# Optimization experiments

Hardware: AMD Instinct MI355X
Metric: run time of the kernel (lower is better)

## Reference

```python
import jax, jax.numpy as jnp
import numpy as np

P, IMG, CH, DM, NL = 16, 224, 3, 512, 6
DI, N, K, R = 2 * DM, 16, 4, DM // 16  # d_inner, d_state, d_conv, dt_rank
BATCH = 32
L = (IMG // P) ** 2
PD = CH * P * P


def layernorm(x, g, b, eps=1e-5):
    mu = x.mean(-1, keepdims=True)
    var = x.var(-1, keepdims=True)
    return (x - mu) / jnp.sqrt(var + eps) * g + b


def mamba_layer(x, inW, convW, convB, xpW, dtW, dtB, A_log, Dvec, outW):
    # x: (B, L, DM)
    Bsz, Ls, _ = x.shape
    xz = x @ inW.T                      # (B, L, 2*DI), in_proj (bias=False)
    xs, z = jnp.split(xz, 2, axis=-1)   # (B, L, DI) each
    # causal depthwise conv1d (kernel K, left pad K-1, truncate to L)
    xp = jnp.pad(xs, ((0, 0), (K - 1, 0), (0, 0)))
    xc = sum(convW[:, k] * xp[:, k:k + Ls, :] for k in range(K)) + convB
    xc = jax.nn.silu(xc)
    # input-dependent dt, B, C
    x_dbl = xc @ xpW.T                  # (B, L, R + 2N)
    dt, Bm, Cm = jnp.split(x_dbl, [R, R + N], axis=-1)
    dt = jax.nn.softplus(dt @ dtW.T + dtB)  # (B, L, DI)
    A = -jnp.exp(A_log)                 # (DI, N)

    def step(h, inp):
        xt, dtt, Bt, Ct = inp           # (B,DI),(B,DI),(B,N),(B,N)
        dA = jnp.exp(dtt[:, :, None] * A)              # (B, DI, N)
        h = dA * h + dtt[:, :, None] * Bt[:, None, :] * xt[:, :, None]
        y = jnp.einsum('bdn,bn->bd', h, Ct)
        return h, y

    h0 = jnp.zeros((Bsz, DI, N), xs.dtype)
    xs_t = jnp.swapaxes(xc, 0, 1)
    dt_t = jnp.swapaxes(dt, 0, 1)
    B_t = jnp.swapaxes(Bm, 0, 1)
    C_t = jnp.swapaxes(Cm, 0, 1)
    _, ys = jax.lax.scan(step, h0, (xs_t, dt_t, B_t, C_t))
    y = jnp.swapaxes(ys, 0, 1) + xc * Dvec   # skip term D*x
    y = y * jax.nn.silu(z)
    return y @ outW.T                    # out_proj (bias=False)


def setup_inputs() -> dict:
    key = jax.random.key(0)
    ks = jax.random.split(key, 16)
    s = 0.02
    inp = {
        'x': jax.random.normal(ks[0], (BATCH, CH, IMG, IMG), jnp.float32),
        'ln0_g': jnp.ones((PD,), jnp.float32),
        'ln0_b': jnp.zeros((PD,), jnp.float32),
        'W_emb': jax.random.normal(ks[1], (DM, PD), jnp.float32) * s,
        'b_emb': jnp.zeros((DM,), jnp.float32),
        'ln1_g': jnp.ones((DM,), jnp.float32),
        'ln1_b': jnp.zeros((DM,), jnp.float32),
        'in_proj_w': jax.random.normal(ks[2], (NL, 2 * DI, DM), jnp.float32) * s,
        'conv_w': jax.random.normal(ks[3], (NL, DI, K), jnp.float32) * 0.1,
        'conv_b': jnp.zeros((NL, DI), jnp.float32),
        'x_proj_w': jax.random.normal(ks[4], (NL, R + 2 * N, DI), jnp.float32) * s,
        'dt_proj_w': jax.random.normal(ks[5], (NL, DI, R), jnp.float32) * s,
        'dt_proj_b': jnp.full((NL, DI), float(np.log(np.expm1(0.01))), jnp.float32),
        'A_log': jnp.tile(jnp.log(jnp.arange(1, N + 1, dtype=jnp.float32)), (NL, DI, 1)),
        'D_p': jnp.ones((NL, DI), jnp.float32),
        'out_proj_w': jax.random.normal(ks[6], (NL, DM, DI), jnp.float32) * s,
        'blk_ln_g': jnp.ones((NL, DM), jnp.float32),
        'blk_ln_b': jnp.zeros((NL, DM), jnp.float32),
        'W_head': jax.random.normal(ks[7], (10, DM), jnp.float32) * s,
        'b_head': jnp.zeros((10,), jnp.float32),
    }
    return inp


def reference(x, ln0_g, ln0_b, W_emb, b_emb, ln1_g, ln1_b, in_proj_w, conv_w,
              conv_b, x_proj_w, dt_proj_w, dt_proj_b, A_log, D_p, out_proj_w,
              blk_ln_g, blk_ln_b, W_head, b_head):
    B = x.shape[0]
    # patchify: b c (h p1) (w p2) -> b (h w) (c p1 p2)
    g = IMG // P
    t = x.reshape(B, CH, g, P, g, P).transpose(0, 2, 4, 1, 3, 5).reshape(B, g * g, PD)
    t = layernorm(t, ln0_g, ln0_b)
    t = t @ W_emb.T + b_emb
    t = layernorm(t, ln1_g, ln1_b)
    for i in range(NL):
        y = mamba_layer(t, in_proj_w[i], conv_w[i], conv_b[i], x_proj_w[i],
                        dt_proj_w[i], dt_proj_b[i], A_log[i], D_p[i], out_proj_w[i])
        t = layernorm(y + t, blk_ln_g[i], blk_ln_b[i])
    pooled = t.mean(axis=1)
    return pooled @ W_head.T + b_head
```

## Files before the change

kernel.cpp:

```cpp
#include <hip/hip_runtime.h>
#include <cstdint>
#include <cstddef>

#define BATCHN 32
#define LSEQ   196
#define DMODEL 512
#define DINNER 1024
#define PDIM   768
#define NSTATE 16
#define RRANK  32
#define NLAYER 6

typedef __bf16 bf16_t;
typedef __bf16 bf16x8 __attribute__((ext_vector_type(8)));
typedef float  f32x4  __attribute__((ext_vector_type(4)));

__device__ __forceinline__ void gl_lds16(const bf16_t* g, bf16_t* l) {
    __builtin_amdgcn_global_load_lds(
        (const __attribute__((address_space(1))) void*)g,
        (__attribute__((address_space(3))) void*)l, 16, 0, 0);
}

__device__ __forceinline__ size_t swz_addr(int row, int c, int KT) {
    return (((size_t)(row >> 4) * KT + (c >> 5)) << 9)
         + (((row & 15) | (((c >> 3) & 3) << 4)) << 3) + (c & 7);
}

__global__ __launch_bounds__(256) void split_kernel(
    const float* __restrict__ src, bf16_t* __restrict__ hi,
    bf16_t* __restrict__ lo, int n)
{
    int i = blockIdx.x * 256 + threadIdx.x;
    if (i < n) {
        float x = src[i];
        bf16_t h = (bf16_t)x;
        hi[i] = h;
        lo[i] = (bf16_t)(x - (float)h);
    }
}

__global__ __launch_bounds__(256) void gemm_mfma3(
    const bf16_t* __restrict__ Ah, const bf16_t* __restrict__ Al,
    const bf16_t* __restrict__ Wh, const bf16_t* __restrict__ Wl,
    float* __restrict__ C, const float* __restrict__ bias,
    int M, int N, int K)
{
    __shared__ bf16_t sBh[2][128 * 32];
    __shared__ bf16_t sBl[2][128 * 32];

    const int bm = blockIdx.y * 128;
    const int bn = blockIdx.x * 128;
    const int kchunk = K / gridDim.z;
    const int kb = blockIdx.z * kchunk;
    const int KT = K >> 5;
    C += (size_t)blockIdx.z * M * N;

    const int tid  = threadIdx.x;
    const int lane = tid & 63;
    const int w    = tid >> 6;
    const int wm   = (w & 1) * 64;
    const int wn   = (w >> 1) * 64;

    const int lrow = lane >> 2;
    const int cg8  = ((lane & 3) ^ ((lane >> 3) & 3)) * 8;
    const size_t brow = (size_t)(bn + w * 32 + lrow) * K + cg8;
    const int llo = w * 1024;

    const int fr  = lane & 15;
    const int fsw = ((lane >> 4) ^ ((lane >> 1) & 3)) * 8;

    const size_t abase = ((size_t)((bm + wm) >> 4) * KT + (kb >> 5)) * 512
                       + (size_t)lane * 8;
    const size_t amt = (size_t)KT * 512;

    f32x4 acc[4][4] = {};

    #pragma unroll
    for (int j = 0; j < 2; ++j) {
        gl_lds16(Wh + brow + (size_t)j * 16 * K + kb, &sBh[0][llo + j * 512]);
        gl_lds16(Wl + brow + (size_t)j * 16 * K + kb, &sBl[0][llo + j * 512]);
    }
    bf16x8 afh[4], afl[4];
    #pragma unroll
    for (int mt = 0; mt < 4; ++mt) {
        afh[mt] = *(const bf16x8*)(Ah + abase + (size_t)mt * amt);
        afl[mt] = *(const bf16x8*)(Al + abase + (size_t)mt * amt);
    }

    const int kiter = kchunk / 32;
    for (int ki = 0; ki < kiter; ++ki) {
        const int buf = ki & 1;
        __syncthreads();

        bf16x8 nfh[4], nfl[4];
        if (ki + 1 < kiter) {
            const size_t ab = abase + (size_t)(ki + 1) * 512;
            #pragma unroll
            for (int mt = 0; mt < 4; ++mt) {
                nfh[mt] = *(const bf16x8*)(Ah + ab + (size_t)mt * amt);
                nfl[mt] = *(const bf16x8*)(Al + ab + (size_t)mt * amt);
            }
            const int k0 = kb + (ki + 1) * 32;
            #pragma unroll
            for (int j = 0; j < 2; ++j) {
                gl_lds16(Wh + brow + (size_t)j * 16 * K + k0,
                         &sBh[buf ^ 1][llo + j * 512]);
                gl_lds16(Wl + brow + (size_t)j * 16 * K + k0,
                         &sBl[buf ^ 1][llo + j * 512]);
            }
        }

        #pragma unroll
        for (int nt = 0; nt < 4; ++nt) {
            const int r = wn + nt * 16 + fr;
            bf16x8 bfh = *(const bf16x8*)&sBh[buf][r * 32 + fsw];
            bf16x8 bfl = *(const bf16x8*)&sBl[buf][r * 32 + fsw];
            #pragma unroll
            for (int mt = 0; mt < 4; ++mt)
                acc[mt][nt] = __builtin_amdgcn_mfma_f32_16x16x32_bf16(
                    afh[mt], bfh, acc[mt][nt], 0, 0, 0);
            #pragma unroll
            for (int mt = 0; mt < 4; ++mt)
                acc[mt][nt] = __builtin_amdgcn_mfma_f32_16x16x32_bf16(
                    afh[mt], bfl, acc[mt][nt], 0, 0, 0);
            #pragma unroll
            for (int mt = 0; mt < 4; ++mt)
                acc[mt][nt] = __builtin_amdgcn_mfma_f32_16x16x32_bf16(
                    afl[mt], bfh, acc[mt][nt], 0, 0, 0);
        }

        if (ki + 1 < kiter) {
            #pragma unroll
            for (int mt = 0; mt < 4; ++mt) {
                afh[mt] = nfh[mt]; afl[mt] = nfl[mt];
            }
        }
    }

    const int cr = (lane >> 4) * 4;
    const int cc = lane & 15;
    #pragma unroll
    for (int nt = 0; nt < 4; ++nt) {
        const int n = bn + wn + nt * 16 + cc;
        const float bv = bias ? bias[n] : 0.f;
        #pragma unroll
        for (int mt = 0; mt < 4; ++mt) {
            const int m0 = bm + wm + mt * 16 + cr;
            #pragma unroll
            for (int r = 0; r < 4; ++r)
                C[(size_t)(m0 + r) * N + n] = acc[mt][nt][r] + bv;
        }
    }
}

__global__ __launch_bounds__(256) void gemm_nt(
    const float* __restrict__ A, int lda,
    const float* __restrict__ W,
    float* __restrict__ C, int ldc,
    const float* __restrict__ bias,
    int M, int N, int K, int act)
{
    __shared__ float As[16][64];
    __shared__ float Ws[16][64];
    const int bm = blockIdx.y * 64;
    const int bn = blockIdx.x * 64;
    const int tid = threadIdx.x;
    const int tx = tid & 15;
    const int ty = tid >> 4;
    const int r   = tid >> 2;
    const int kk4 = (tid & 3) << 2;

    float acc[4][4];
    #pragma unroll
    for (int i = 0; i < 4; ++i)
        #pragma unroll
        for (int j = 0; j < 4; ++j) acc[i][j] = 0.f;

    for (int k0 = 0; k0 < K; k0 += 16) {
        float4 va = *(const float4*)(A + (size_t)(bm + r) * lda + k0 + kk4);
        float4 vw = *(const float4*)(W + (size_t)(bn + r) * K   + k0 + kk4);
        __syncthreads();
        As[kk4 + 0][r] = va.x; As[kk4 + 1][r] = va.y;
        As[kk4 + 2][r] = va.z; As[kk4 + 3][r] = va.w;
        Ws[kk4 + 0][r] = vw.x; Ws[kk4 + 1][r] = vw.y;
        Ws[kk4 + 2][r] = vw.z; Ws[kk4 + 3][r] = vw.w;
        __syncthreads();
        #pragma unroll
        for (int kk = 0; kk < 16; ++kk) {
            float4 a = *(const float4*)&As[kk][ty << 2];
            float4 b = *(const float4*)&Ws[kk][tx << 2];
            acc[0][0] += a.x * b.x; acc[0][1] += a.x * b.y;
            acc[0][2] += a.x * b.z; acc[0][3] += a.x * b.w;
            acc[1][0] += a.y * b.x; acc[1][1] += a.y * b.y;
            acc[1][2] += a.y * b.z; acc[1][3] += a.y * b.w;
            acc[2][0] += a.z * b.x; acc[2][1] += a.z * b.y;
            acc[2][2] += a.z * b.z; acc[2][3] += a.z * b.w;
            acc[3][0] += a.w * b.x; acc[3][1] += a.w * b.y;
            acc[3][2] += a.w * b.z; acc[3][3] += a.w * b.w;
        }
    }

    #pragma unroll
    for (int i = 0; i < 4; ++i) {
        const int m = bm + (ty << 2) + i;
        #pragma unroll
        for (int j = 0; j < 4; ++j) {
            const int n = bn + (tx << 2) + j;
            float v = acc[i][j];
            if (bias) v += bias[n];
            if (act == 1) {
                v = (v > 20.f) ? v : log1pf(expf(v));
            }
            C[(size_t)m * ldc + n] = v;
        }
    }
}

__global__ __launch_bounds__(256) void conv_xproj_kernel(
    const float* __restrict__ xz, const float* __restrict__ cw,
    const float* __restrict__ cb, const float* __restrict__ xpW,
    float* __restrict__ xc, float* __restrict__ Cpart,
    int kchunk)
{
    __shared__ float As[16][64];
    __shared__ float Ws[16][64];
    __shared__ float scw[128 * 4 + 128];

    const int bm = blockIdx.y * 64;
    const int kb = blockIdx.z * kchunk;
    Cpart += (size_t)blockIdx.z * (BATCHN * LSEQ) * 64;

    const int tid = threadIdx.x;
    if (tid < 128) {
        *(float4*)&scw[tid * 4] = *(const float4*)(cw + (size_t)(kb + tid) * 4);
        scw[512 + tid] = cb[kb + tid];
    }
    __syncthreads();

    const int tx = tid & 15;
    const int ty = tid >> 4;
    const int r   = tid >> 2;
    const int kk4 = (tid & 3) << 2;
    const int bl  = bm + r;
    const int l   = bl % LSEQ;
    const float* xrow = xz + ((size_t)bl << 11);

    float acc[4][4];
    #pragma unroll
    for (int i = 0; i < 4; ++i)
        #pragma unroll
        for (int j = 0; j < 4; ++j) acc[i][j] = 0.f;

    for (int k0 = 0; k0 < kchunk; k0 += 16) {
        const int cl = k0 + kk4;
        const int c  = kb + cl;
        float4 va = *(const float4*)&scw[512 + cl];
        #pragma unroll
        for (int kk = 0; kk < 4; ++kk) {
            int ls = l + kk - 3;
            if (ls >= 0) {
                float4 xv = *(const float4*)(xrow + ((ptrdiff_t)(kk - 3) << 11) + c);
                va.x += scw[(cl + 0) * 4 + kk] * xv.x;
                va.y += scw[(cl + 1) * 4 + kk] * xv.y;
                va.z += scw[(cl + 2) * 4 + kk] * xv.z;
                va.w += scw[(cl + 3) * 4 + kk] * xv.w;
            }
        }
        va.x = va.x * __builtin_amdgcn_rcpf(1.f + __expf(-va.x));
        va.y = va.y * __builtin_amdgcn_rcpf(1.f + __expf(-va.y));
        va.z = va.z * __builtin_amdgcn_rcpf(1.f + __expf(-va.z));
        va.w = va.w * __builtin_amdgcn_rcpf(1.f + __expf(-va.w));
        *(float4*)(xc + ((size_t)bl << 10) + c) = va;

        float4 vw = *(const float4*)(xpW + (size_t)r * DINNER + c);
        __syncthreads();
        As[kk4 + 0][r] = va.x; As[kk4 + 1][r] = va.y;
        As[kk4 + 2][r] = va.z; As[kk4 + 3][r] = va.w;
        Ws[kk4 + 0][r] = vw.x; Ws[kk4 + 1][r] = vw.y;
        Ws[kk4 + 2][r] = vw.z; Ws[kk4 + 3][r] = vw.w;
        __syncthreads();
        #pragma unroll
        for (int kk = 0; kk < 16; ++kk) {
            float4 a = *(const float4*)&As[kk][ty << 2];
            float4 b = *(const float4*)&Ws[kk][tx << 2];
            acc[0][0] += a.x * b.x; acc[0][1] += a.x * b.y;
            acc[0][2] += a.x * b.z; acc[0][3] += a.x * b.w;
            acc[1][0] += a.y * b.x; acc[1][1] += a.y * b.y;
            acc[1][2] += a.y * b.z; acc[1][3] += a.y * b.w;
            acc[2][0] += a.z * b.x; acc[2][1] += a.z * b.y;
            acc[2][2] += a.z * b.z; acc[2][3] += a.z * b.w;
            acc[3][0] += a.w * b.x; acc[3][1] += a.w * b.y;
            acc[3][2] += a.w * b.z; acc[3][3] += a.w * b.w;
        }
    }

    #pragma unroll
    for (int i = 0; i < 4; ++i) {
        const int m = bm + (ty << 2) + i;
        #pragma unroll
        for (int j = 0; j < 4; ++j) {
            const int n = (tx << 2) + j;
            Cpart[(size_t)m * 64 + n] = acc[i][j];
        }
    }
}

__global__ __launch_bounds__(256) void reduce_splitk(
    const float* __restrict__ part, float* __restrict__ out, int n, int nsplit)
{
    int i = blockIdx.x * 256 + threadIdx.x;
    if (i < n) {
        float s = 0.f;
        for (int j = 0; j < nsplit; ++j) s += part[(size_t)j * n + i];
        out[i] = s;
    }
}

__global__ __launch_bounds__(256) void patchify_kernel(
    const float* __restrict__ x, float* __restrict__ tp)
{
    int idx = blockIdx.x * 256 + threadIdx.x;
    int pd = idx % PDIM;
    int bl = idx / PDIM;
    int l = bl % LSEQ, b = bl / LSEQ;
    int c = pd >> 8, rem = pd & 255, p1 = rem >> 4, p2 = rem & 15;
    int gh = l / 14, gw = l % 14;
    int hh = gh * 16 + p1, ww = gw * 16 + p2;
    tp[idx] = x[(((size_t)b * 3 + c) * 224 + hh) * 224 + ww];
}

__global__ __launch_bounds__(256) void ln_kernel(
    const float* __restrict__ in, const float* __restrict__ in2,
    const float* __restrict__ res,
    const float* __restrict__ g, const float* __restrict__ bt,
    float* __restrict__ out, bf16_t* __restrict__ hi,
    bf16_t* __restrict__ lo, int W)
{
    __shared__ float red[4];
    const int row = blockIdx.x;
    const size_t base = (size_t)row * W;
    const int nper = W >> 8;
    const int KT = W >> 5;
    float vals[3];
    float s = 0.f;
    for (int j = 0; j < nper; ++j) {
        int c = (j << 8) + threadIdx.x;
        float v = in[base + c];
        if (in2) v += in2[base + c];
        if (res) v += res[base + c];
        vals[j] = v;
        s += v;
    }
    int lane = threadIdx.x & 63, wid = threadIdx.x >> 6;
    #pragma unroll
    for (int o = 32; o > 0; o >>= 1) s += __shfl_down(s, o);
    if (lane == 0) red[wid] = s;
    __syncthreads();
    float mu = (red[0] + red[1] + red[2] + red[3]) / (float)W;
    __syncthreads();
    float vs = 0.f;
    for (int j = 0; j < nper; ++j) { float d = vals[j] - mu; vs += d * d; }
    #pragma unroll
    for (int o = 32; o > 0; o >>= 1) vs += __shfl_down(vs, o);
    if (lane == 0) red[wid] = vs;
    __syncthreads();
    float var = (red[0] + red[1] + red[2] + red[3]) / (float)W;
    float rstd = rsqrtf(var + 1e-5f);
    for (int j = 0; j < nper; ++j) {
        int c = (j << 8) + threadIdx.x;
        float v = (vals[j] - mu) * rstd * g[c] + bt[c];
        if (out) out[base + c] = v;
        if (hi) {
            bf16_t h = (bf16_t)v;
            const size_t a = swz_addr(row, c, KT);
            hi[a] = h;
            lo[a] = (bf16_t)(v - (float)h);
        }
    }
}

template<int J>
__device__ __forceinline__ float qbcast(float v) {
    constexpr int ctrl = J | (J << 2) | (J << 4) | (J << 6);
    return __int_as_float(__builtin_amdgcn_mov_dpp(
        __float_as_int(v), ctrl, 0xF, 0xF, true));
}

__global__ __launch_bounds__(256, 1) void scan_kernel(
    const float* __restrict__ xc, const float* __restrict__ dt,
    const float* __restrict__ xdbl, const float* __restrict__ A_log,
    const float* __restrict__ Dv, const float* __restrict__ xz,
    bf16_t* __restrict__ yh, bf16_t* __restrict__ yl)
{
    __shared__ float sBC[4][2][256];

    const int b    = blockIdx.y;
    const int tid  = threadIdx.x;
    const int lane = tid & 63;
    const int w    = tid >> 6;
    const int q    = tid >> 2;
    const int sub  = tid & 3;
    const int d    = blockIdx.x * 64 + q;

    float A2[4], h[4];
    #pragma unroll
    for (int n = 0; n < 4; ++n) {
        A2[n] = -__expf(A_log[d * NSTATE + sub * 4 + n]) * 1.44269504f;
        h[n] = 0.f;
    }
    const float Dval = Dv[d];
    const size_t bL = (size_t)b * LSEQ;

    const float* pdt = dt + (bL + sub) * DINNER + d;
    const float* pxc = xc + (bL + sub) * DINNER + d;
    const float* pz  = xz + ((bL + sub) << 11) + DINNER + d;

    const float* xrow = xdbl + bL * 64;
    const int roff = (lane >> 4) * 64 + (lane & 15) * 4;
    float* lds0 = &sBC[w][0][0];
    float* lds1 = &sBC[w][1][0];

    float4 r0 = *(const float4*)(xrow + roff);
    float4 r1 = *(const float4*)(xrow + 256 + roff);
    float4 rowreg = *(const float4*)(xrow + 512 + roff);
    *(float4*)(lds0 + roff) = r0;
    *(float4*)(lds1 + roff) = r1;

    float dt_c = pdt[0];          float xc_c = pxc[0];          float z_c = pz[0];
    float dt_1 = pdt[4 * DINNER]; float xc_1 = pxc[4 * DINNER]; float z_1 = pz[4 * 2048];

    for (int g = 0; g < 49; ++g) {
        const int gl  = (g + 3 <= 48) ? g + 3 : 48;
        float4 rownext = *(const float4*)(xrow + gl * 256 + roff);
        const int adv = (g < 47) ? 2 : (48 - g);
        float dt_2 = pdt[(size_t)adv * 4 * DINNER];
        float xc_2 = pxc[(size_t)adv * 4 * DINNER];
        float z_2  = pz[(size_t)adv * 4 * 2048];

        const float* Bbuf = (g & 1) ? lds1 : lds0;
        float acc_keep = 0.f;

#define SCAN_STEP(J) do {                                                     \
        float4 Bv = *(const float4*)&Bbuf[(J) * 64 + 32 + 4 * sub];           \
        float4 Cv = *(const float4*)&Bbuf[(J) * 64 + 48 + 4 * sub];           \
        float dtv = qbcast<J>(dt_c);                                          \
        float xv  = qbcast<J>(xc_c);                                          \
        float dtx = dtv * xv;                                                 \
        h[0] = exp2f(dtv * A2[0]) * h[0] + dtx * Bv.x;                        \
        h[1] = exp2f(dtv * A2[1]) * h[1] + dtx * Bv.y;                        \
        h[2] = exp2f(dtv * A2[2]) * h[2] + dtx * Bv.z;                        \
        h[3] = exp2f(dtv * A2[3]) * h[3] + dtx * Bv.w;                        \
        float acc = h[0] * Cv.x + h[1] * Cv.y + h[2] * Cv.z + h[3] * Cv.w;    \
        acc += __shfl_xor(acc, 1);                                            \
        acc += __shfl_xor(acc, 2);                                            \
        acc_keep = (sub == (J)) ? acc : acc_keep;                             \
    } while (0)

        SCAN_STEP(0);
        SCAN_STEP(1);
        SCAN_STEP(2);
        SCAN_STEP(3);
#undef SCAN_STEP

        {
            float yv = acc_keep + xc_c * Dval;
            float sz = z_c * __builtin_amdgcn_rcpf(1.f + __expf(-z_c));
            float o  = yv * sz;
            bf16_t ho = (bf16_t)o;
            const int row = (int)bL + 4 * g + sub;
            const size_t oi = swz_addr(row, d, DINNER >> 5);
            yh[oi] = ho;
            yl[oi] = (bf16_t)(o - (float)ho);
        }

        *(float4*)(((g & 1) ? lds1 : lds0) + roff) = rowreg;
        rowreg = rownext;

        pdt += 4 * DINNER; pxc += 4 * DINNER; pz += 4 * 2048;
        dt_c = dt_1; xc_c = xc_1; z_c = z_1;
        dt_1 = dt_2; xc_1 = xc_2; z_1 = z_2;
    }
}

__global__ __launch_bounds__(256) void pool_kernel(
    const float* __restrict__ t, float* __restrict__ pooled)
{
    int idx = blockIdx.x * 256 + threadIdx.x;
    int dm = idx & (DMODEL - 1);
    int b = idx >> 9;
    float s = 0.f;
    for (int l = 0; l < LSEQ; ++l)
        s += t[((size_t)(b * LSEQ + l) << 9) + dm];
    pooled[idx] = s * (1.f / (float)LSEQ);
}

__global__ __launch_bounds__(320) void head_kernel(
    const float* __restrict__ pooled, const float* __restrict__ Wh,
    const float* __restrict__ bh, float* __restrict__ out)
{
    int tid = threadIdx.x;
    if (tid >= 320) return;
    int b = tid / 10, o = tid % 10;
    float s = bh[o];
    for (int k = 0; k < DMODEL; ++k)
        s += pooled[b * DMODEL + k] * Wh[o * DMODEL + k];
    out[b * 10 + o] = s;
}

extern "C" void kernel_launch(void* const* d_in, const int* in_sizes, int n_in,
                              void* d_out, int out_size, void* d_ws, size_t ws_size,
                              hipStream_t stream)
{
    const float* x         = (const float*)d_in[0];
    const float* ln0_g     = (const float*)d_in[1];
    const float* ln0_b     = (const float*)d_in[2];
    const float* W_emb     = (const float*)d_in[3];
    const float* b_emb     = (const float*)d_in[4];
    const float* ln1_g     = (const float*)d_in[5];
    const float* ln1_b     = (const float*)d_in[6];
    const float* in_proj_w = (const float*)d_in[7];
    const float* conv_w    = (const float*)d_in[8];
    const float* conv_b    = (const float*)d_in[9];
    const float* x_proj_w  = (const float*)d_in[10];
    const float* dt_proj_w = (const float*)d_in[11];
    const float* dt_proj_b = (const float*)d_in[12];
    const float* A_log     = (const float*)d_in[13];
    const float* D_p       = (const float*)d_in[14];
    const float* out_proj_w= (const float*)d_in[15];
    const float* blk_ln_g  = (const float*)d_in[16];
    const float* blk_ln_b  = (const float*)d_in[17];
    const float* W_head    = (const float*)d_in[18];
    const float* b_head    = (const float*)d_in[19];

    const int M = BATCHN * LSEQ;
    const int NSPLIT = 8;

    char* ws = (char*)d_ws;
    size_t off = 0;
    auto alloc = [&](size_t bytes) -> void* {
        void* p = (void*)(ws + off);
        off += (bytes + 255) & ~(size_t)255;
        return p;
    };
    float*  tp     = (float*)alloc((size_t)M * PDIM * 4);
    bf16_t* tp_h   = (bf16_t*)alloc((size_t)M * PDIM * 2);
    bf16_t* tp_l   = (bf16_t*)alloc((size_t)M * PDIM * 2);
    float*  t      = (float*)alloc((size_t)M * DMODEL * 4);
    bf16_t* t_h    = (bf16_t*)alloc((size_t)M * DMODEL * 2);
    bf16_t* t_l    = (bf16_t*)alloc((size_t)M * DMODEL * 2);
    float*  xz     = (float*)alloc((size_t)M * 2 * DINNER * 4);
    float*  xc     = (float*)alloc((size_t)M * DINNER * 4);
    float*  xdbl   = (float*)alloc((size_t)M * 64 * 4);
    float*  dtbuf  = (float*)alloc((size_t)M * DINNER * 4);
    bf16_t* y_h    = (bf16_t*)alloc((size_t)M * DINNER * 2);
    bf16_t* y_l    = (bf16_t*)alloc((size_t)M * DINNER * 2);
    float*  pooled = (float*)alloc((size_t)BATCHN * DMODEL * 4);
    float*  xdbl_p = tp;
    float*  yout   = dtbuf;
    const int n_inW  = NLAYER * 2 * DINNER * DMODEL;
    const int n_outW = NLAYER * DMODEL * DINNER;
    const int n_embW = DMODEL * PDIM;
    bf16_t* winh  = (bf16_t*)alloc((size_t)n_inW * 2);
    bf16_t* winl  = (bf16_t*)alloc((size_t)n_inW * 2);
    bf16_t* wouth = (bf16_t*)alloc((size_t)n_outW * 2);
    bf16_t* woutl = (bf16_t*)alloc((size_t)n_outW * 2);
    bf16_t* wembh = (bf16_t*)alloc((size_t)n_embW * 2);
    bf16_t* wembl = (bf16_t*)alloc((size_t)n_embW * 2);
    (void)ws_size; (void)in_sizes; (void)n_in; (void)out_size;

    split_kernel<<<(n_inW  + 255) / 256, 256, 0, stream>>>(in_proj_w,  winh,  winl,  n_inW);
    split_kernel<<<(n_outW + 255) / 256, 256, 0, stream>>>(out_proj_w, wouth, woutl, n_outW);
    split_kernel<<<(n_embW + 255) / 256, 256, 0, stream>>>(W_emb,      wembh, wembl, n_embW);

    patchify_kernel<<<(M * PDIM) / 256, 256, 0, stream>>>(x, tp);
    ln_kernel<<<M, 256, 0, stream>>>(tp, nullptr, nullptr, ln0_g, ln0_b,
                                     nullptr, tp_h, tp_l, PDIM);
    gemm_mfma3<<<dim3(DMODEL / 128, M / 128, 1), 256, 0, stream>>>(
        tp_h, tp_l, wembh, wembl, t, b_emb, M, DMODEL, PDIM);
    ln_kernel<<<M, 256, 0, stream>>>(t, nullptr, nullptr, ln1_g, ln1_b,
                                     t, t_h, t_l, DMODEL);

    for (int i = 0; i < NLAYER; ++i) {
        const bf16_t* winh_i  = winh  + (size_t)i * 2 * DINNER * DMODEL;
        const bf16_t* winl_i  = winl  + (size_t)i * 2 * DINNER * DMODEL;
        const bf16_t* wouth_i = wouth + (size_t)i * DMODEL * DINNER;
        const bf16_t* woutl_i = woutl + (size_t)i * DMODEL * DINNER;
        const float* cw   = conv_w    + (size_t)i * DINNER * 4;
        const float* cb   = conv_b    + (size_t)i * DINNER;
        const float* xpW  = x_proj_w  + (size_t)i * 64 * DINNER;
        const float* dtW  = dt_proj_w + (size_t)i * DINNER * RRANK;
        const float* dtB  = dt_proj_b + (size_t)i * DINNER;
        const float* Ali  = A_log     + (size_t)i * DINNER * NSTATE;
        const float* Di   = D_p       + (size_t)i * DINNER;
        const float* bg   = blk_ln_g  + (size_t)i * DMODEL;
        const float* bb   = blk_ln_b  + (size_t)i * DMODEL;

        gemm_mfma3<<<dim3((2 * DINNER) / 128, M / 128, 1), 256, 0, stream>>>(
            t_h, t_l, winh_i, winl_i, xz, nullptr, M, 2 * DINNER, DMODEL);
        conv_xproj_kernel<<<dim3(1, M / 64, NSPLIT), 256, 0, stream>>>(
            xz, cw, cb, xpW, xc, xdbl_p, DINNER / NSPLIT);
        reduce_splitk<<<(M * 64 + 255) / 256, 256, 0, stream>>>(
            xdbl_p, xdbl, M * 64, NSPLIT);
        gemm_nt<<<dim3(DINNER / 64, M / 64), 256, 0, stream>>>(
            xdbl, 64, dtW, dtbuf, DINNER, dtB, M, DINNER, RRANK, 1);
        scan_kernel<<<dim3(DINNER / 64, BATCHN), 256, 0, stream>>>(
            xc, dtbuf, xdbl, Ali, Di, xz, y_h, y_l);
        gemm_mfma3<<<dim3(DMODEL / 128, M / 128, 2), 256, 0, stream>>>(
            y_h, y_l, wouth_i, woutl_i, yout, nullptr, M, DMODEL, DINNER);
        ln_kernel<<<M, 256, 0, stream>>>(yout, yout + (size_t)M * DMODEL, t,
                                         bg, bb, t, t_h, t_l, DMODEL);
    }

    pool_kernel<<<(BATCHN * DMODEL) / 256, 256, 0, stream>>>(t, pooled);
    head_kernel<<<1, 320, 0, stream>>>(pooled, W_head, b_head, (float*)d_out);
}
```

Measured before the change: 1.562 ms.

## Give each wave private triple-buffered LDS B tiles and drop block barriers

```diff
diff --git a/kernel.cpp b/kernel.cpp
--- a/kernel.cpp
+++ b/kernel.cpp
@@ -45,8 +45,7 @@
     float* __restrict__ C, const float* __restrict__ bias,
     int M, int N, int K)
 {
-    __shared__ bf16_t sBh[2][128 * 32];
-    __shared__ bf16_t sBl[2][128 * 32];
+    __shared__ bf16_t sB[4 * 3 * 2048];
 
     const int bm = blockIdx.y * 128;
     const int bn = blockIdx.x * 128;
@@ -58,94 +57,88 @@
     const int tid  = threadIdx.x;
     const int lane = tid & 63;
     const int w    = tid >> 6;
-    const int wm   = (w & 1) * 64;
-    const int wn   = (w >> 1) * 64;
+    const int wn   = w * 32;
 
     const int lrow = lane >> 2;
     const int cg8  = ((lane & 3) ^ ((lane >> 3) & 3)) * 8;
-    const size_t brow = (size_t)(bn + w * 32 + lrow) * K + cg8;
-    const int llo = w * 1024;
+    const size_t brow = (size_t)(bn + wn + lrow) * K + cg8;
+    const int wbase = w * 6144;
 
     const int fr  = lane & 15;
     const int fsw = ((lane >> 4) ^ ((lane >> 1) & 3)) * 8;
 
-    const size_t abase = ((size_t)((bm + wm) >> 4) * KT + (kb >> 5)) * 512
+    const size_t abase = ((size_t)(bm >> 4) * KT + (kb >> 5)) * 512
                        + (size_t)lane * 8;
     const size_t amt = (size_t)KT * 512;
 
-    f32x4 acc[4][4] = {};
-
-    #pragma unroll
-    for (int j = 0; j < 2; ++j) {
-        gl_lds16(Wh + brow + (size_t)j * 16 * K + kb, &sBh[0][llo + j * 512]);
-        gl_lds16(Wl + brow + (size_t)j * 16 * K + kb, &sBl[0][llo + j * 512]);
-    }
-    bf16x8 afh[4], afl[4];
-    #pragma unroll
-    for (int mt = 0; mt < 4; ++mt) {
-        afh[mt] = *(const bf16x8*)(Ah + abase + (size_t)mt * amt);
-        afl[mt] = *(const bf16x8*)(Al + abase + (size_t)mt * amt);
-    }
+    f32x4 acc[8][2] = {};
 
     const int kiter = kchunk / 32;
+
+    #pragma unroll
+    for (int p = 0; p < 2; ++p) {
+        const int k0 = kb + p * 32;
+        bf16_t* dst = &sB[wbase + p * 2048];
+        #pragma unroll
+        for (int j = 0; j < 2; ++j) {
+            gl_lds16(Wh + brow + (size_t)j * 16 * K + k0, dst + j * 512);
+            gl_lds16(Wl + brow + (size_t)j * 16 * K + k0, dst + 1024 + j * 512);
+        }
+    }
+
     for (int ki = 0; ki < kiter; ++ki) {
-        const int buf = ki & 1;
-        __syncthreads();
-
-        bf16x8 nfh[4], nfl[4];
-        if (ki + 1 < kiter) {
-            const size_t ab = abase + (size_t)(ki + 1) * 512;
-            #pragma unroll
-            for (int mt = 0; mt < 4; ++mt) {
-                nfh[mt] = *(const bf16x8*)(Ah + ab + (size_t)mt * amt);
-                nfl[mt] = *(const bf16x8*)(Al + ab + (size_t)mt * amt);
-            }
-            const int k0 = kb + (ki + 1) * 32;
+        bf16x8 afh[8], afl[8];
+        const size_t ab = abase + (size_t)ki * 512;
+        #pragma unroll
+        for (int mt = 0; mt < 8; ++mt) {
+            afh[mt] = *(const bf16x8*)(Ah + ab + (size_t)mt * amt);
+            afl[mt] = *(const bf16x8*)(Al + ab + (size_t)mt * amt);
+        }
+
+        if (ki + 2 < kiter) {
+            const int k0 = kb + (ki + 2) * 32;
+            bf16_t* dst = &sB[wbase + ((ki + 2) % 3) * 2048];
             #pragma unroll
             for (int j = 0; j < 2; ++j) {
-                gl_lds16(Wh + brow + (size_t)j * 16 * K + k0,
-                         &sBh[buf ^ 1][llo + j * 512]);
-                gl_lds16(Wl + brow + (size_t)j * 16 * K + k0,
-                         &sBl[buf ^ 1][llo + j * 512]);
+                gl_lds16(Wh + brow + (size_t)j * 16 * K + k0, dst + j * 512);
+                gl_lds16(Wl + brow + (size_t)j * 16 * K + k0, dst + 1024 + j * 512);
             }
         }
 
-        #pragma unroll
-        for (int nt = 0; nt < 4; ++nt) {
-            const int r = wn + nt * 16 + fr;
-            bf16x8 bfh = *(const bf16x8*)&sBh[buf][r * 32 + fsw];
-            bf16x8 bfl = *(const bf16x8*)&sBl[buf][r * 32 + fsw];
+        const bf16_t* src = &sB[wbase + (ki % 3) * 2048];
+        bf16x8 bfh[2], bfl[2];
+        #pragma unroll
+        for (int nt = 0; nt < 2; ++nt) {
+            bfh[nt] = *(const bf16x8*)(src + nt * 512 + fr * 32 + fsw);
+            bfl[nt] = *(const bf16x8*)(src + 1024 + nt * 512 + fr * 32 + fsw);
+        }
+
+        #pragma unroll
+        for (int nt = 0; nt < 2; ++nt) {
             #pragma unroll
-            for (int mt = 0; mt < 4; ++mt)
+            for (int mt = 0; mt < 8; ++mt)
                 acc[mt][nt] = __builtin_amdgcn_mfma_f32_16x16x32_bf16(
-                    afh[mt], bfh, acc[mt][nt], 0, 0, 0);
+                    afh[mt], bfh[nt], acc[mt][nt], 0, 0, 0);
             #pragma unroll
-            for (int mt = 0; mt < 4; ++mt)
+            for (int mt = 0; mt < 8; ++mt)
                 acc[mt][nt] = __builtin_amdgcn_mfma_f32_16x16x32_bf16(
-                    afh[mt], bfl, acc[mt][nt], 0, 0, 0);
+                    afh[mt], bfl[nt], acc[mt][nt], 0, 0, 0);
             #pragma unroll
-            for (int mt = 0; mt < 4; ++mt)
+            for (int mt = 0; mt < 8; ++mt)
                 acc[mt][nt] = __builtin_amdgcn_mfma_f32_16x16x32_bf16(
-                    afl[mt], bfh, acc[mt][nt], 0, 0, 0);
-        }
-
-        if (ki + 1 < kiter) {
-            #pragma unroll
-            for (int mt = 0; mt < 4; ++mt) {
-                afh[mt] = nfh[mt]; afl[mt] = nfl[mt];
-            }
+                    afl[mt], bfh[nt], acc[mt][nt], 0, 0, 0);
         }
     }
 
     const int cr = (lane >> 4) * 4;
     const int cc = lane & 15;
     #pragma unroll
-    for (int nt = 0; nt < 4; ++nt) {
+    for (int nt = 0; nt < 2; ++nt) {
         const int n = bn + wn + nt * 16 + cc;
         const float bv = bias ? bias[n] : 0.f;
         #pragma unroll
-        for (int mt = 0; mt < 4; ++mt) {
-            const int m0 = bm + wm + mt * 16 + cr;
+        for (int mt = 0; mt < 8; ++mt) {
+            const int m0 = bm + mt * 16 + cr;
             #pragma unroll
             for (int r = 0; r < 4; ++r)
                 C[(size_t)(m0 + r) * N + n] = acc[mt][nt][r] + bv;
```

Result: slower. 1.603 ms (+2.6%).
